# Performance work log

Measured on AMD Instinct MI355X. Metric: run time of the kernel, lower is better.

## Reference

```python
import jax, jax.numpy as jnp
import numpy as np

E, P, D, U = 500000, 4000000, 64, 64


def setup_inputs() -> dict:
    key = jax.random.key(0)
    k1, k2, k3 = jax.random.split(key, 3)
    edges_sph_features = jax.random.normal(k1, (E, D), dtype=jnp.float32)
    edges_neighbor = jax.random.randint(k2, (P, 2), 0, E, dtype=jnp.int32)
    kernel = jax.random.normal(k3, (D, U), dtype=jnp.float32) * 0.05
    bias = jnp.zeros((U,), dtype=jnp.float32)
    return {
        "edges_sph_features": edges_sph_features,
        "edges_neighbor": edges_neighbor,
        "kernel": kernel,
        "bias": bias,
    }


def reference(edges_sph_features, edges_neighbor, kernel, bias):
    # gather neighbor edge features: [P, D]
    gathered = jnp.take(edges_sph_features, edges_neighbor[:, 1], axis=0)
    # scatter-reduce by receiving edge id: [E, D]
    num_segments = edges_sph_features.shape[0]
    aggregated = jax.ops.segment_sum(gathered, edges_neighbor[:, 0],
                                     num_segments=num_segments)
    # linear transform (note: original call() does NOT apply the activation)
    return aggregated @ kernel + bias
```

## Files before the change

### kernel.cpp

```cpp
#include <hip/hip_runtime.h>


#define FD 64
#define BKT_SHIFT 10
#define BKT_MAX 512
#define TILE_A 8192
#define CAP_B 12288


__global__ __launch_bounds__(256) void k_bhist(const int2* __restrict__ nbr,
                                               int* __restrict__ bcnt, int P) {
    __shared__ int h[BKT_MAX];
    const int t = threadIdx.x;
    for (int i = t; i < BKT_MAX; i += 256) h[i] = 0;
    __syncthreads();
    const int base = blockIdx.x * 4096;
#pragma unroll
    for (int j = 0; j < 16; ++j) {
        int p = base + j * 256 + t;
        if (p < P) atomicAdd(&h[nbr[p].x >> BKT_SHIFT], 1);
    }
    __syncthreads();
    for (int i = t; i < BKT_MAX; i += 256) {
        int v = h[i];
        if (v) atomicAdd(&bcnt[i], v);
    }
}

__global__ __launch_bounds__(512) void k_bscan(const int* __restrict__ bcnt,
                                               int* __restrict__ bbase,
                                               int* __restrict__ bcur,
                                               int NBKT, int P) {
    __shared__ int s[BKT_MAX];
    const int t = threadIdx.x;
    s[t] = (t < NBKT) ? bcnt[t] : 0;
    __syncthreads();
    int orig = s[t];
    for (int off = 1; off < BKT_MAX; off <<= 1) {
        int v = (t >= off) ? s[t - off] : 0;
        __syncthreads();
        s[t] += v;
        __syncthreads();
    }
    int ex = s[t] - orig;
    if (t < NBKT) {
        bbase[t] = ex;
        bcur[t] = ex;
    }
    if (t == NBKT - 1) bbase[NBKT] = s[t];
    (void)P;
}

__global__ __launch_bounds__(256) void k_partition(const int2* __restrict__ nbr,
                                                   int* __restrict__ bcur,
                                                   int* __restrict__ part, int P) {
    __shared__ int hist[BKT_MAX];
    __shared__ int off[BKT_MAX];
    __shared__ int curs[BKT_MAX];
    __shared__ int rb[BKT_MAX];
    __shared__ int tsum[256];
    __shared__ int stage_v[TILE_A];
    __shared__ unsigned short stage_b[TILE_A];

    const int t = threadIdx.x;
    const int base = blockIdx.x * TILE_A;

    for (int i = t; i < BKT_MAX; i += 256) hist[i] = 0;
    __syncthreads();

#pragma unroll
    for (int j = 0; j < TILE_A / 256; ++j) {
        int p = base + j * 256 + t;
        if (p < P) atomicAdd(&hist[nbr[p].x >> BKT_SHIFT], 1);
    }
    __syncthreads();

    int h0 = hist[2 * t], h1 = hist[2 * t + 1];
    int pairsum = h0 + h1;
    tsum[t] = pairsum;
    __syncthreads();
    for (int o = 1; o < 256; o <<= 1) {
        int v = (t >= o) ? tsum[t - o] : 0;
        __syncthreads();
        tsum[t] += v;
        __syncthreads();
    }
    int ex = tsum[t] - pairsum;
    off[2 * t] = ex;
    off[2 * t + 1] = ex + h0;
    curs[2 * t] = ex;
    curs[2 * t + 1] = ex + h0;
    __syncthreads();

    for (int i = t; i < BKT_MAX; i += 256) {
        int c = hist[i];
        rb[i] = c ? atomicAdd(&bcur[i], c) : 0;
    }
#pragma unroll
    for (int j = 0; j < TILE_A / 256; ++j) {
        int p = base + j * 256 + t;
        if (p < P) {
            int2 e = nbr[p];
            int b = e.x >> BKT_SHIFT;
            int v = (e.y << BKT_SHIFT) | (e.x & ((1 << BKT_SHIFT) - 1));
            int pos = atomicAdd(&curs[b], 1);
            stage_v[pos] = v;
            stage_b[pos] = (unsigned short)b;
        }
    }
    __syncthreads();

    int n = min(TILE_A, P - base);
    for (int idx = t; idx < n; idx += 256) {
        int b = stage_b[idx];
        part[rb[b] + (idx - off[b])] = stage_v[idx];
    }
}

__global__ __launch_bounds__(256) void k_bucket(const int* __restrict__ part,
                                                const int* __restrict__ bbase,
                                                int* __restrict__ offs,
                                                int* __restrict__ csr,
                                                int E, int P, int NBKT) {
    __shared__ int hist[1 << BKT_SHIFT];
    __shared__ int cur[1 << BKT_SHIFT];
    __shared__ int tsum[256];
    __shared__ int stage[CAP_B];

    const int b = blockIdx.x;
    const int t = threadIdx.x;
    const int base = bbase[b];
    const int n = bbase[b + 1] - base;
    const int ND = 1 << BKT_SHIFT;

    for (int i = t; i < ND; i += 256) hist[i] = 0;
    __syncthreads();

    for (int idx = t; idx < n; idx += 256)
        atomicAdd(&hist[part[base + idx] & (ND - 1)], 1);
    __syncthreads();

    int h[4];
    int s = 0;
#pragma unroll
    for (int j = 0; j < 4; ++j) {
        h[j] = hist[4 * t + j];
        s += h[j];
    }
    tsum[t] = s;
    __syncthreads();
    for (int o = 1; o < 256; o <<= 1) {
        int v = (t >= o) ? tsum[t - o] : 0;
        __syncthreads();
        tsum[t] += v;
        __syncthreads();
    }
    int run = tsum[t] - s;
#pragma unroll
    for (int j = 0; j < 4; ++j) {
        int d = (b << BKT_SHIFT) + 4 * t + j;
        cur[4 * t + j] = run;
        if (d < E) offs[d] = base + run;
        run += h[j];
    }
    if (b == NBKT - 1 && t == 0) offs[E] = P;
    __syncthreads();

    if (n <= CAP_B) {
        for (int idx = t; idx < n; idx += 256) {
            int v = part[base + idx];
            int p = atomicAdd(&cur[v & (ND - 1)], 1);
            stage[p] = v >> BKT_SHIFT;
        }
        __syncthreads();
        for (int idx = t; idx < n; idx += 256) csr[base + idx] = stage[idx];
    } else {
        for (int idx = t; idx < n; idx += 256) {
            int v = part[base + idx];
            int p = atomicAdd(&cur[v & (ND - 1)], 1);
            csr[base + p] = v >> BKT_SHIFT;
        }
    }
}


__global__ __launch_bounds__(256) void k_agg(const float* __restrict__ feat,
                                             const int* __restrict__ offs,
                                             const int* __restrict__ csr,
                                             const float* __restrict__ Kmat,
                                             const float* __restrict__ bias,
                                             float* __restrict__ out, int E) {
    __shared__ float xr[4][FD];
    const int lane = threadIdx.x & 63;
    const int wid = threadIdx.x >> 6;
    const int g = lane >> 4;
    const int gl = lane & 15;

    float kcol[FD];
#pragma unroll
    for (int d = 0; d < FD; ++d) kcol[d] = Kmat[d * FD + lane];
    const float b = bias[lane];

    const int wv = __builtin_amdgcn_readfirstlane((int)blockIdx.x * 4 + wid);
    const int nw = (int)gridDim.x * 4;
    float4* const xw4 = (float4*)&xr[wid][0];

    for (int e = wv; e < E; e += nw) {
        const int beg = offs[e], end = offs[e + 1];
        float4 a = {0.f, 0.f, 0.f, 0.f};
        int i = beg;
        for (; i + 8 <= end; i += 8) {
            int s0 = csr[i + g];
            int s1 = csr[i + 4 + g];
            const float4 v0 =
                *(const float4*)&feat[(size_t)s0 * FD + 4 * gl];
            const float4 v1 =
                *(const float4*)&feat[(size_t)s1 * FD + 4 * gl];
            a.x += v0.x + v1.x;
            a.y += v0.y + v1.y;
            a.z += v0.z + v1.z;
            a.w += v0.w + v1.w;
        }
        for (; i < end; i += 4) {
            int idx = i + g;
            if (idx < end) {
                int s = csr[idx];
                const float4 v =
                    *(const float4*)&feat[(size_t)s * FD + 4 * gl];
                a.x += v.x;
                a.y += v.y;
                a.z += v.z;
                a.w += v.w;
            }
        }
        a.x += __shfl_xor(a.x, 16, 64);
        a.y += __shfl_xor(a.y, 16, 64);
        a.z += __shfl_xor(a.z, 16, 64);
        a.w += __shfl_xor(a.w, 16, 64);
        a.x += __shfl_xor(a.x, 32, 64);
        a.y += __shfl_xor(a.y, 32, 64);
        a.z += __shfl_xor(a.z, 32, 64);
        a.w += __shfl_xor(a.w, 32, 64);

        if (g == 0) xw4[gl] = a;
        float o = b;
        const float4* xp = (const float4*)&xr[wid][0];
#pragma unroll
        for (int j = 0; j < FD / 4; ++j) {
            float4 q = xp[j];
            o += q.x * kcol[4 * j + 0] + q.y * kcol[4 * j + 1] +
                 q.z * kcol[4 * j + 2] + q.w * kcol[4 * j + 3];
        }
        __builtin_nontemporal_store(o, &out[(size_t)e * FD + lane]);
    }
}


__global__ __launch_bounds__(256) void k_hist(const int* __restrict__ nbr,
                                              int* __restrict__ cnt, int P) {
    int p = blockIdx.x * 256 + threadIdx.x;
    if (p < P) atomicAdd(&cnt[nbr[2 * p]], 1);
}

__global__ __launch_bounds__(256) void k_blocksum(const int* __restrict__ cnt,
                                                  int* __restrict__ bsum, int E) {
    int base = blockIdx.x * 1024;
    int t = threadIdx.x;
    int s = 0;
#pragma unroll
    for (int j = 0; j < 4; ++j) {
        int e = base + t + j * 256;
        if (e < E) s += cnt[e];
    }
    for (int off = 32; off; off >>= 1) s += __shfl_down(s, off, 64);
    __shared__ int wsum[4];
    int wid = t >> 6, lane = t & 63;
    if (lane == 0) wsum[wid] = s;
    __syncthreads();
    if (t == 0) bsum[blockIdx.x] = wsum[0] + wsum[1] + wsum[2] + wsum[3];
}

__global__ __launch_bounds__(1024) void k_scan_bsum(int* bsum, int NB) {
    __shared__ int s[1024];
    int t = threadIdx.x;
    s[t] = (t < NB) ? bsum[t] : 0;
    __syncthreads();
    int orig = s[t];
    for (int off = 1; off < 1024; off <<= 1) {
        int v = (t >= off) ? s[t - off] : 0;
        __syncthreads();
        s[t] += v;
        __syncthreads();
    }
    if (t < NB) bsum[t] = s[t] - orig;
}

__global__ __launch_bounds__(256) void k_scan_write(const int* __restrict__ cnt,
                                                    const int* __restrict__ boff,
                                                    int* __restrict__ offs,
                                                    int* __restrict__ cur,
                                                    int E) {
    __shared__ int tsum[256];
    int b = blockIdx.x, t = threadIdx.x;
    int base = b * 1024 + t * 4;
    int c[4];
#pragma unroll
    for (int j = 0; j < 4; ++j) {
        int e = base + j;
        c[j] = (e < E) ? cnt[e] : 0;
    }
    int local = c[0] + c[1] + c[2] + c[3];
    tsum[t] = local;
    __syncthreads();
    for (int off = 1; off < 256; off <<= 1) {
        int v = (t >= off) ? tsum[t - off] : 0;
        __syncthreads();
        tsum[t] += v;
        __syncthreads();
    }
    int run = tsum[t] - local + boff[b];
#pragma unroll
    for (int j = 0; j < 4; ++j) {
        int e = base + j;
        if (e < E) {
            offs[e] = run;
            cur[e] = run;
            run += c[j];
            if (e == E - 1) offs[E] = run;
        }
    }
}

__global__ __launch_bounds__(256) void k_build(const int* __restrict__ nbr,
                                               int* __restrict__ cur,
                                               int* __restrict__ csr, int P) {
    int p = blockIdx.x * 256 + threadIdx.x;
    if (p < P) {
        int dst = nbr[2 * p + 0];
        int src = nbr[2 * p + 1];
        int pos = atomicAdd(&cur[dst], 1);
        csr[pos] = src;
    }
}


__global__ __launch_bounds__(256) void ea_scatter(const float* __restrict__ feat,
                                                  const int* __restrict__ nbr,
                                                  float* __restrict__ agg, int P) {
    const int lane = threadIdx.x & 63;
    const int pair = __builtin_amdgcn_readfirstlane(
        (int)blockIdx.x * 4 + ((int)threadIdx.x >> 6));
    if (pair < P) {
        const int dst = nbr[2 * pair + 0];
        const int src = nbr[2 * pair + 1];
        atomicAdd(&agg[(size_t)dst * FD + lane], feat[(size_t)src * FD + lane]);
    }
}

__global__ __launch_bounds__(256) void ea_transform(float* __restrict__ io,
                                                    const float* __restrict__ Kmat,
                                                    const float* __restrict__ bias,
                                                    int E) {
    const int lane = threadIdx.x & 63;
    float kcol[FD];
#pragma unroll
    for (int d = 0; d < FD; ++d) kcol[d] = Kmat[d * FD + lane];
    const float b = bias[lane];
    const int wv = __builtin_amdgcn_readfirstlane(
        (int)blockIdx.x * 4 + ((int)threadIdx.x >> 6));
    const int nw = (int)gridDim.x * 4;
    for (int e = wv; e < E; e += nw) {
        const float* __restrict__ row = io + (size_t)e * FD;
        float acc = b;
#pragma unroll
        for (int d = 0; d < FD; ++d) acc += row[d] * kcol[d];
        io[(size_t)e * FD + lane] = acc;
    }
}


extern "C" void kernel_launch(void* const* d_in, const int* in_sizes, int n_in,
                              void* d_out, int out_size, void* d_ws, size_t ws_size,
                              hipStream_t stream) {
    const float* feat = (const float*)d_in[0];
    const int* nbr = (const int*)d_in[1];
    const float* Kmat = (const float*)d_in[2];
    const float* bias = (const float*)d_in[3];
    float* out = (float*)d_out;

    const int E = in_sizes[0] / FD;
    const int P = in_sizes[1] / 2;
    const int NBKT = (E + (1 << BKT_SHIFT) - 1) >> BKT_SHIFT;
    const int NB = (E + 1023) / 1024;

    const size_t need_new =
        ((size_t)(E + 1) + (BKT_MAX + 1) + BKT_MAX + 2 * (size_t)P) * sizeof(int);
    const size_t need_old =
        ((size_t)E + (size_t)(E + 1) + 1024 + (size_t)P) * sizeof(int);

    if (NBKT <= BKT_MAX && ws_size >= need_new) {
        int* offs = (int*)d_ws;
        int* bbase = offs + (E + 1);
        int* bcur = bbase + (BKT_MAX + 1);
        int* part = bcur + BKT_MAX;
        int* csr = part + P;

        hipMemsetAsync(bcur, 0, BKT_MAX * sizeof(int), stream);
        k_bhist<<<(P + 4095) / 4096, 256, 0, stream>>>((const int2*)nbr, bcur, P);
        k_bscan<<<1, BKT_MAX, 0, stream>>>(bcur, bbase, bcur, NBKT, P);
        k_partition<<<(P + TILE_A - 1) / TILE_A, 256, 0, stream>>>(
            (const int2*)nbr, bcur, part, P);
        k_bucket<<<NBKT, 256, 0, stream>>>(part, bbase, offs, csr, E, P, NBKT);
        k_agg<<<4096, 256, 0, stream>>>(feat, offs, csr, Kmat, bias, out, E);
    } else if (ws_size >= need_old && NB <= 1024) {
        int* cur = (int*)d_ws;
        int* offs = cur + E;
        int* bsum = offs + E + 1;
        int* csr = bsum + 1024;

        hipMemsetAsync(cur, 0, (size_t)E * sizeof(int), stream);
        k_hist<<<(P + 255) / 256, 256, 0, stream>>>(nbr, cur, P);
        k_blocksum<<<NB, 256, 0, stream>>>(cur, bsum, E);
        k_scan_bsum<<<1, 1024, 0, stream>>>(bsum, NB);
        k_scan_write<<<NB, 256, 0, stream>>>(cur, bsum, offs, cur, E);
        k_build<<<(P + 255) / 256, 256, 0, stream>>>(nbr, cur, csr, P);
        k_agg<<<4096, 256, 0, stream>>>(feat, offs, csr, Kmat, bias, out, E);
    } else {
        hipMemsetAsync(d_out, 0, (size_t)out_size * sizeof(float), stream);
        ea_scatter<<<(P + 3) / 4, 256, 0, stream>>>(feat, nbr, out, P);
        ea_transform<<<2048, 256, 0, stream>>>(out, Kmat, bias, E);
    }
}
```

Measured before the change: 534.4 us.

## Software-pipeline offset and CSR index loads across iterations in aggregation kernel

The aggregation loop now prefetches the row offsets two iterations ahead and the first 16 CSR neighbor indices one iteration ahead. The first 16 neighbors of each row are then gathered without waiting on the index load. This targets the dependent latency chain offs to csr to feat that each wave used to stall on. In exchange it uses more registers and issues clamped extra CSR loads whose values are discarded when a row has fewer than 16 neighbors.

```diff
diff --git a/kernel.cpp b/kernel.cpp
--- a/kernel.cpp
+++ b/kernel.cpp
@@ -189,7 +189,8 @@
                                              const int* __restrict__ csr,
                                              const float* __restrict__ Kmat,
                                              const float* __restrict__ bias,
-                                             float* __restrict__ out, int E) {
+                                             float* __restrict__ out,
+                                             int E, int P) {
     __shared__ float xr[4][FD];
     const int lane = threadIdx.x & 63;
     const int wid = threadIdx.x >> 6;
@@ -204,35 +205,73 @@
     const int wv = __builtin_amdgcn_readfirstlane((int)blockIdx.x * 4 + wid);
     const int nw = (int)gridDim.x * 4;
     float4* const xw4 = (float4*)&xr[wid][0];
-
-    for (int e = wv; e < E; e += nw) {
-        const int beg = offs[e], end = offs[e + 1];
+    const int Pm1 = P - 1;
+
+    int e = wv;
+    if (e >= E) return;
+
+    int beg0 = offs[e], end0 = offs[e + 1];
+    int beg1 = 0, end1 = 0;
+    if (e + nw < E) {
+        beg1 = offs[e + nw];
+        end1 = offs[e + nw + 1];
+    }
+    int s0p = csr[min(beg0 + g, Pm1)];
+    int s1p = csr[min(beg0 + 4 + g, Pm1)];
+    int s2p = csr[min(beg0 + 8 + g, Pm1)];
+    int s3p = csr[min(beg0 + 12 + g, Pm1)];
+
+    for (; e < E; e += nw) {
+        int e2 = e + 2 * nw;
+        int beg2 = 0, end2 = 0;
+        if (e2 < E) {
+            beg2 = offs[e2];
+            end2 = offs[e2 + 1];
+        }
+        int t0 = 0, t1 = 0, t2 = 0, t3 = 0;
+        if (e + nw < E) {
+            t0 = csr[min(beg1 + g, Pm1)];
+            t1 = csr[min(beg1 + 4 + g, Pm1)];
+            t2 = csr[min(beg1 + 8 + g, Pm1)];
+            t3 = csr[min(beg1 + 12 + g, Pm1)];
+        }
+
         float4 a = {0.f, 0.f, 0.f, 0.f};
-        int i = beg;
-        for (; i + 8 <= end; i += 8) {
-            int s0 = csr[i + g];
-            int s1 = csr[i + 4 + g];
-            const float4 v0 =
-                *(const float4*)&feat[(size_t)s0 * FD + 4 * gl];
-            const float4 v1 =
-                *(const float4*)&feat[(size_t)s1 * FD + 4 * gl];
+        if (beg0 + g < end0) {
+            const float4 v = *(const float4*)&feat[(size_t)s0p * FD + 4 * gl];
+            a.x += v.x; a.y += v.y; a.z += v.z; a.w += v.w;
+        }
+        if (beg0 + 4 + g < end0) {
+            const float4 v = *(const float4*)&feat[(size_t)s1p * FD + 4 * gl];
+            a.x += v.x; a.y += v.y; a.z += v.z; a.w += v.w;
+        }
+        if (beg0 + 8 + g < end0) {
+            const float4 v = *(const float4*)&feat[(size_t)s2p * FD + 4 * gl];
+            a.x += v.x; a.y += v.y; a.z += v.z; a.w += v.w;
+        }
+        if (beg0 + 12 + g < end0) {
+            const float4 v = *(const float4*)&feat[(size_t)s3p * FD + 4 * gl];
+            a.x += v.x; a.y += v.y; a.z += v.z; a.w += v.w;
+        }
+        int i = beg0 + 16;
+        for (; i + 8 <= end0; i += 8) {
+            int s0 = csr[i + g], s1 = csr[i + 4 + g];
+            const float4 v0 = *(const float4*)&feat[(size_t)s0 * FD + 4 * gl];
+            const float4 v1 = *(const float4*)&feat[(size_t)s1 * FD + 4 * gl];
             a.x += v0.x + v1.x;
             a.y += v0.y + v1.y;
             a.z += v0.z + v1.z;
             a.w += v0.w + v1.w;
         }
-        for (; i < end; i += 4) {
+        for (; i < end0; i += 4) {
             int idx = i + g;
-            if (idx < end) {
+            if (idx < end0) {
                 int s = csr[idx];
-                const float4 v =
-                    *(const float4*)&feat[(size_t)s * FD + 4 * gl];
-                a.x += v.x;
-                a.y += v.y;
-                a.z += v.z;
-                a.w += v.w;
+                const float4 v = *(const float4*)&feat[(size_t)s * FD + 4 * gl];
+                a.x += v.x; a.y += v.y; a.z += v.z; a.w += v.w;
             }
         }
+
         a.x += __shfl_xor(a.x, 16, 64);
         a.y += __shfl_xor(a.y, 16, 64);
         a.z += __shfl_xor(a.z, 16, 64);
@@ -252,6 +291,10 @@
                  q.z * kcol[4 * j + 2] + q.w * kcol[4 * j + 3];
         }
         __builtin_nontemporal_store(o, &out[(size_t)e * FD + lane]);
+
+        beg0 = beg1; end0 = end1;
+        beg1 = beg2; end1 = end2;
+        s0p = t0; s1p = t1; s2p = t2; s3p = t3;
     }
 }
 
@@ -411,7 +454,7 @@
         k_partition<<<(P + TILE_A - 1) / TILE_A, 256, 0, stream>>>(
             (const int2*)nbr, bcur, part, P);
         k_bucket<<<NBKT, 256, 0, stream>>>(part, bbase, offs, csr, E, P, NBKT);
-        k_agg<<<4096, 256, 0, stream>>>(feat, offs, csr, Kmat, bias, out, E);
+        k_agg<<<4096, 256, 0, stream>>>(feat, offs, csr, Kmat, bias, out, E, P);
     } else if (ws_size >= need_old && NB <= 1024) {
         int* cur = (int*)d_ws;
         int* offs = cur + E;
@@ -424,7 +467,7 @@
         k_scan_bsum<<<1, 1024, 0, stream>>>(bsum, NB);
         k_scan_write<<<NB, 256, 0, stream>>>(cur, bsum, offs, cur, E);
         k_build<<<(P + 255) / 256, 256, 0, stream>>>(nbr, cur, csr, P);
-        k_agg<<<4096, 256, 0, stream>>>(feat, offs, csr, Kmat, bias, out, E);
+        k_agg<<<4096, 256, 0, stream>>>(feat, offs, csr, Kmat, bias, out, E, P);
     } else {
         hipMemsetAsync(d_out, 0, (size_t)out_size * sizeof(float), stream);
         ea_scatter<<<(P + 3) / 4, 256, 0, stream>>>(feat, nbr, out, P);
```

Measured after the change: 542.9 us. About the same (+1.6%).

## Fuse bucket CSR build and aggregation into LDS-accumulating per-bucket kernel

Applied to the files above, without the earlier changes.

Drops the per-bucket CSR construction kernel and the separate CSR-driven aggregation kernel. A single fused kernel now assigns each block half of a 1024-destination bucket, gathers source feature rows straight from the partitioned pair list, and accumulates them into a 128KB LDS tile with shared-memory float atomics. It then applies the 64x64 linear transform and writes the output. This removes the CSR write and re-read plus one launch. In exchange, both halves of each bucket scan the whole bucket, and the large LDS footprint limits residency to about one 512-thread block per CU, which may hurt latency hiding for the random gathers.

```diff
diff --git a/kernel.cpp b/kernel.cpp
--- a/kernel.cpp
+++ b/kernel.cpp
@@ -5,7 +5,7 @@
 #define BKT_SHIFT 10
 #define BKT_MAX 512
 #define TILE_A 8192
-#define CAP_B 12288
+#define NDH 512
 
 
 __global__ __launch_bounds__(256) void k_bhist(const int2* __restrict__ nbr,
@@ -117,72 +117,165 @@
     }
 }
 
-__global__ __launch_bounds__(256) void k_bucket(const int* __restrict__ part,
-                                                const int* __restrict__ bbase,
-                                                int* __restrict__ offs,
-                                                int* __restrict__ csr,
-                                                int E, int P, int NBKT) {
-    __shared__ int hist[1 << BKT_SHIFT];
-    __shared__ int cur[1 << BKT_SHIFT];
+
+__global__ __launch_bounds__(512) void k_fused(const float* __restrict__ feat,
+                                               const int* __restrict__ part,
+                                               const int* __restrict__ bbase,
+                                               const float* __restrict__ Kmat,
+                                               const float* __restrict__ bias,
+                                               float* __restrict__ out, int E) {
+    __shared__ float accf[NDH * FD];
+    __shared__ int pst_all[8 * 64];
+
+    const int tid = threadIdx.x;
+    const int lane = tid & 63;
+    const int wid = tid >> 6;
+    const int b = (int)blockIdx.x >> 1;
+    const int half = (int)blockIdx.x & 1;
+
+    float4 z = {0.f, 0.f, 0.f, 0.f};
+    float4* ap = (float4*)accf;
+#pragma unroll
+    for (int i = 0; i < (NDH * FD / 4) / 512; ++i) ap[tid + i * 512] = z;
+
+    float kcol[FD];
+#pragma unroll
+    for (int d = 0; d < FD; ++d) kcol[d] = Kmat[d * FD + lane];
+    const float bb = bias[lane];
+
+    __syncthreads();
+
+    const int rb = bbase[b], re = bbase[b + 1];
+    int* const pst = pst_all + wid * 64;
+
+    for (int c = rb + wid * 64; c < re; c += 512) {
+        int idx = c + lane;
+        int pv = (idx < re) ? part[idx] : (int)0x80000000;
+        pst[lane] = pv;
+#pragma unroll
+        for (int j = 0; j < 64; j += 8) {
+            int4 qa = *(const int4*)(pst + j);
+            int4 qb = *(const int4*)(pst + j + 4);
+            int pvs[8] = {qa.x, qa.y, qa.z, qa.w, qb.x, qb.y, qb.z, qb.w};
+            float f[8];
+            bool v[8];
+#pragma unroll
+            for (int k = 0; k < 8; ++k) {
+                int p = pvs[k];
+                v[k] = (p >= 0) && (((p >> 9) & 1) == half);
+                if (v[k]) f[k] = feat[(size_t)(p >> 10) * FD + lane];
+            }
+#pragma unroll
+            for (int k = 0; k < 8; ++k)
+                if (v[k]) atomicAdd(&accf[(pvs[k] & (NDH - 1)) * FD + lane], f[k]);
+        }
+    }
+
+    __syncthreads();
+
+    const int d0 = (b << BKT_SHIFT) + half * NDH;
+    for (int dl = wid; dl < NDH; dl += 8) {
+        int d = d0 + dl;
+        if (d >= E) break;
+        float o = bb;
+        const float4* xp = (const float4*)&accf[dl * FD];
+#pragma unroll
+        for (int j = 0; j < FD / 4; ++j) {
+            float4 q = xp[j];
+            o += q.x * kcol[4 * j + 0] + q.y * kcol[4 * j + 1] +
+                 q.z * kcol[4 * j + 2] + q.w * kcol[4 * j + 3];
+        }
+        __builtin_nontemporal_store(o, &out[(size_t)d * FD + lane]);
+    }
+}
+
+
+__global__ __launch_bounds__(256) void k_hist(const int* __restrict__ nbr,
+                                              int* __restrict__ cnt, int P) {
+    int p = blockIdx.x * 256 + threadIdx.x;
+    if (p < P) atomicAdd(&cnt[nbr[2 * p]], 1);
+}
+
+__global__ __launch_bounds__(256) void k_blocksum(const int* __restrict__ cnt,
+                                                  int* __restrict__ bsum, int E) {
+    int base = blockIdx.x * 1024;
+    int t = threadIdx.x;
+    int s = 0;
+#pragma unroll
+    for (int j = 0; j < 4; ++j) {
+        int e = base + t + j * 256;
+        if (e < E) s += cnt[e];
+    }
+    for (int off = 32; off; off >>= 1) s += __shfl_down(s, off, 64);
+    __shared__ int wsum[4];
+    int wid = t >> 6, lane = t & 63;
+    if (lane == 0) wsum[wid] = s;
+    __syncthreads();
+    if (t == 0) bsum[blockIdx.x] = wsum[0] + wsum[1] + wsum[2] + wsum[3];
+}
+
+__global__ __launch_bounds__(1024) void k_scan_bsum(int* bsum, int NB) {
+    __shared__ int s[1024];
+    int t = threadIdx.x;
+    s[t] = (t < NB) ? bsum[t] : 0;
+    __syncthreads();
+    int orig = s[t];
+    for (int off = 1; off < 1024; off <<= 1) {
+        int v = (t >= off) ? s[t - off] : 0;
+        __syncthreads();
+        s[t] += v;
+        __syncthreads();
+    }
+    if (t < NB) bsum[t] = s[t] - orig;
+}
+
+__global__ __launch_bounds__(256) void k_scan_write(const int* __restrict__ cnt,
+                                                    const int* __restrict__ boff,
+                                                    int* __restrict__ offs,
+                                                    int* __restrict__ cur,
+                                                    int E) {
     __shared__ int tsum[256];
-    __shared__ int stage[CAP_B];
-
-    const int b = blockIdx.x;
-    const int t = threadIdx.x;
-    const int base = bbase[b];
-    const int n = bbase[b + 1] - base;
-    const int ND = 1 << BKT_SHIFT;
-
-    for (int i = t; i < ND; i += 256) hist[i] = 0;
-    __syncthreads();
-
-    for (int idx = t; idx < n; idx += 256)
-        atomicAdd(&hist[part[base + idx] & (ND - 1)], 1);
-    __syncthreads();
-
-    int h[4];
-    int s = 0;
+    int b = blockIdx.x, t = threadIdx.x;
+    int base = b * 1024 + t * 4;
+    int c[4];
 #pragma unroll
     for (int j = 0; j < 4; ++j) {
-        h[j] = hist[4 * t + j];
-        s += h[j];
-    }
-    tsum[t] = s;
-    __syncthreads();
-    for (int o = 1; o < 256; o <<= 1) {
-        int v = (t >= o) ? tsum[t - o] : 0;
+        int e = base + j;
+        c[j] = (e < E) ? cnt[e] : 0;
+    }
+    int local = c[0] + c[1] + c[2] + c[3];
+    tsum[t] = local;
+    __syncthreads();
+    for (int off = 1; off < 256; off <<= 1) {
+        int v = (t >= off) ? tsum[t - off] : 0;
         __syncthreads();
         tsum[t] += v;
         __syncthreads();
     }
-    int run = tsum[t] - s;
+    int run = tsum[t] - local + boff[b];
 #pragma unroll
     for (int j = 0; j < 4; ++j) {
-        int d = (b << BKT_SHIFT) + 4 * t + j;
-        cur[4 * t + j] = run;
-        if (d < E) offs[d] = base + run;
-        run += h[j];
-    }
-    if (b == NBKT - 1 && t == 0) offs[E] = P;
-    __syncthreads();
-
-    if (n <= CAP_B) {
-        for (int idx = t; idx < n; idx += 256) {
-            int v = part[base + idx];
-            int p = atomicAdd(&cur[v & (ND - 1)], 1);
-            stage[p] = v >> BKT_SHIFT;
-        }
-        __syncthreads();
-        for (int idx = t; idx < n; idx += 256) csr[base + idx] = stage[idx];
-    } else {
-        for (int idx = t; idx < n; idx += 256) {
-            int v = part[base + idx];
-            int p = atomicAdd(&cur[v & (ND - 1)], 1);
-            csr[base + p] = v >> BKT_SHIFT;
-        }
-    }
-}
-
+        int e = base + j;
+        if (e < E) {
+            offs[e] = run;
+            cur[e] = run;
+            run += c[j];
+            if (e == E - 1) offs[E] = run;
+        }
+    }
+}
+
+__global__ __launch_bounds__(256) void k_build(const int* __restrict__ nbr,
+                                               int* __restrict__ cur,
+                                               int* __restrict__ csr, int P) {
+    int p = blockIdx.x * 256 + threadIdx.x;
+    if (p < P) {
+        int dst = nbr[2 * p + 0];
+        int src = nbr[2 * p + 1];
+        int pos = atomicAdd(&cur[dst], 1);
+        csr[pos] = src;
+    }
+}
 
 __global__ __launch_bounds__(256) void k_agg(const float* __restrict__ feat,
                                              const int* __restrict__ offs,
@@ -210,12 +303,9 @@
         float4 a = {0.f, 0.f, 0.f, 0.f};
         int i = beg;
         for (; i + 8 <= end; i += 8) {
-            int s0 = csr[i + g];
-            int s1 = csr[i + 4 + g];
-            const float4 v0 =
-                *(const float4*)&feat[(size_t)s0 * FD + 4 * gl];
-            const float4 v1 =
-                *(const float4*)&feat[(size_t)s1 * FD + 4 * gl];
+            int s0 = csr[i + g], s1 = csr[i + 4 + g];
+            const float4 v0 = *(const float4*)&feat[(size_t)s0 * FD + 4 * gl];
+            const float4 v1 = *(const float4*)&feat[(size_t)s1 * FD + 4 * gl];
             a.x += v0.x + v1.x;
             a.y += v0.y + v1.y;
             a.z += v0.z + v1.z;
@@ -225,12 +315,8 @@
             int idx = i + g;
             if (idx < end) {
                 int s = csr[idx];
-                const float4 v =
-                    *(const float4*)&feat[(size_t)s * FD + 4 * gl];
-                a.x += v.x;
-                a.y += v.y;
-                a.z += v.z;
-                a.w += v.w;
+                const float4 v = *(const float4*)&feat[(size_t)s * FD + 4 * gl];
+                a.x += v.x; a.y += v.y; a.z += v.z; a.w += v.w;
             }
         }
         a.x += __shfl_xor(a.x, 16, 64);
@@ -252,94 +338,6 @@
                  q.z * kcol[4 * j + 2] + q.w * kcol[4 * j + 3];
         }
         __builtin_nontemporal_store(o, &out[(size_t)e * FD + lane]);
-    }
-}
-
-
-__global__ __launch_bounds__(256) void k_hist(const int* __restrict__ nbr,
-                                              int* __restrict__ cnt, int P) {
-    int p = blockIdx.x * 256 + threadIdx.x;
-    if (p < P) atomicAdd(&cnt[nbr[2 * p]], 1);
-}
-
-__global__ __launch_bounds__(256) void k_blocksum(const int* __restrict__ cnt,
-                                                  int* __restrict__ bsum, int E) {
-    int base = blockIdx.x * 1024;
-    int t = threadIdx.x;
-    int s = 0;
-#pragma unroll
-    for (int j = 0; j < 4; ++j) {
-        int e = base + t + j * 256;
-        if (e < E) s += cnt[e];
-    }
-    for (int off = 32; off; off >>= 1) s += __shfl_down(s, off, 64);
-    __shared__ int wsum[4];
-    int wid = t >> 6, lane = t & 63;
-    if (lane == 0) wsum[wid] = s;
-    __syncthreads();
-    if (t == 0) bsum[blockIdx.x] = wsum[0] + wsum[1] + wsum[2] + wsum[3];
-}
-
-__global__ __launch_bounds__(1024) void k_scan_bsum(int* bsum, int NB) {
-    __shared__ int s[1024];
-    int t = threadIdx.x;
-    s[t] = (t < NB) ? bsum[t] : 0;
-    __syncthreads();
-    int orig = s[t];
-    for (int off = 1; off < 1024; off <<= 1) {
-        int v = (t >= off) ? s[t - off] : 0;
-        __syncthreads();
-        s[t] += v;
-        __syncthreads();
-    }
-    if (t < NB) bsum[t] = s[t] - orig;
-}
-
-__global__ __launch_bounds__(256) void k_scan_write(const int* __restrict__ cnt,
-                                                    const int* __restrict__ boff,
-                                                    int* __restrict__ offs,
-                                                    int* __restrict__ cur,
-                                                    int E) {
-    __shared__ int tsum[256];
-    int b = blockIdx.x, t = threadIdx.x;
-    int base = b * 1024 + t * 4;
-    int c[4];
-#pragma unroll
-    for (int j = 0; j < 4; ++j) {
-        int e = base + j;
-        c[j] = (e < E) ? cnt[e] : 0;
-    }
-    int local = c[0] + c[1] + c[2] + c[3];
-    tsum[t] = local;
-    __syncthreads();
-    for (int off = 1; off < 256; off <<= 1) {
-        int v = (t >= off) ? tsum[t - off] : 0;
-        __syncthreads();
-        tsum[t] += v;
-        __syncthreads();
-    }
-    int run = tsum[t] - local + boff[b];
-#pragma unroll
-    for (int j = 0; j < 4; ++j) {
-        int e = base + j;
-        if (e < E) {
-            offs[e] = run;
-            cur[e] = run;
-            run += c[j];
-            if (e == E - 1) offs[E] = run;
-        }
-    }
-}
-
-__global__ __launch_bounds__(256) void k_build(const int* __restrict__ nbr,
-                                               int* __restrict__ cur,
-                                               int* __restrict__ csr, int P) {
-    int p = blockIdx.x * 256 + threadIdx.x;
-    if (p < P) {
-        int dst = nbr[2 * p + 0];
-        int src = nbr[2 * p + 1];
-        int pos = atomicAdd(&cur[dst], 1);
-        csr[pos] = src;
     }
 }
 
@@ -394,7 +392,7 @@
     const int NB = (E + 1023) / 1024;
 
     const size_t need_new =
-        ((size_t)(E + 1) + (BKT_MAX + 1) + BKT_MAX + 2 * (size_t)P) * sizeof(int);
+        ((size_t)(E + 1) + (BKT_MAX + 1) + BKT_MAX + (size_t)P) * sizeof(int);
     const size_t need_old =
         ((size_t)E + (size_t)(E + 1) + 1024 + (size_t)P) * sizeof(int);
 
@@ -403,15 +401,13 @@
         int* bbase = offs + (E + 1);
         int* bcur = bbase + (BKT_MAX + 1);
         int* part = bcur + BKT_MAX;
-        int* csr = part + P;
 
         hipMemsetAsync(bcur, 0, BKT_MAX * sizeof(int), stream);
         k_bhist<<<(P + 4095) / 4096, 256, 0, stream>>>((const int2*)nbr, bcur, P);
         k_bscan<<<1, BKT_MAX, 0, stream>>>(bcur, bbase, bcur, NBKT, P);
         k_partition<<<(P + TILE_A - 1) / TILE_A, 256, 0, stream>>>(
             (const int2*)nbr, bcur, part, P);
-        k_bucket<<<NBKT, 256, 0, stream>>>(part, bbase, offs, csr, E, P, NBKT);
-        k_agg<<<4096, 256, 0, stream>>>(feat, offs, csr, Kmat, bias, out, E);
+        k_fused<<<2 * NBKT, 512, 0, stream>>>(feat, part, bbase, Kmat, bias, out, E);
     } else if (ws_size >= need_old && NB <= 1024) {
         int* cur = (int*)d_ws;
         int* offs = cur + E;
```

Result: slower. 1.740 ms (+225.5%).
